# Optimization experiments

Hardware: AMD Instinct MI355X
Metric: run time of the kernel (lower is better)

## Reference

```python
import jax, jax.numpy as jnp
import numpy as np

D_MODEL = 256
D_INNER = 512
D_STATE = 16
DT_RANK = 16
D_CONV = 4
N_LAYERS = 2
EPS = 1e-5
SEQ_LEN = 16384
IN_DIM = 32
OUT_DIM = 1


def _layernorm(x, g, b):
    m = jnp.mean(x, axis=-1, keepdims=True)
    v = jnp.mean((x - m) ** 2, axis=-1, keepdims=True)
    return (x - m) * jax.lax.rsqrt(v + EPS) * g + b


def _rmsnorm(x, w):
    return x * jax.lax.rsqrt(jnp.mean(x * x, axis=-1, keepdims=True) + EPS) * w


def _selective_scan(x, delta, A, B, C, D):
    # x, delta: (B,L,ED); A: (ED,N); B,C: (B,L,N); D: (ED,)
    dA = jnp.exp(delta[..., None] * A)                    # (B,L,ED,N)
    dBx = (delta * x)[..., None] * B[:, :, None, :]       # (B,L,ED,N)

    def comb(l, r):
        al, bl = l
        ar, br = r
        return (al * ar, bl * ar + br)

    _, hs = jax.lax.associative_scan(comb, (dA, dBx), axis=1)  # (B,L,ED,N)
    y = jnp.einsum('blen,bln->ble', hs, C) + x * D
    return y


def _mamba_block(u, rms_w, inW, convW, convB, xpW, dtW, dtB, A_log, Dp, outW):
    h = _rmsnorm(u, rms_w)
    xz = h @ inW                                   # (B,L,2*ED)
    xin, z = jnp.split(xz, 2, axis=-1)
    # depthwise causal conv1d over time
    xc = jax.lax.conv_general_dilated(
        jnp.transpose(xin, (0, 2, 1)), convW,
        window_strides=(1,), padding=[(D_CONV - 1, 0)],
        feature_group_count=D_INNER,
        dimension_numbers=('NCH', 'OIH', 'NCH')) + convB[None, :, None]
    xs = jax.nn.silu(jnp.transpose(xc, (0, 2, 1)))  # (B,L,ED)
    dbc = xs @ xpW                                  # (B,L,dt_rank+2N)
    delta = jax.nn.softplus(dbc[..., :DT_RANK] @ dtW + dtB)
    Bm = dbc[..., DT_RANK:DT_RANK + D_STATE]
    Cm = dbc[..., DT_RANK + D_STATE:]
    y = _selective_scan(xs, delta, -jnp.exp(A_log), Bm, Cm, Dp)
    out = (y * jax.nn.silu(z)) @ outW
    return u + out  # residual


def _forward(x, W_in, b_in, ln1_g, ln1_b,
             rms_w, inW, convW, convB, xpW, dtW, dtB, A_log, Dp, outW,
             ln2_g, ln2_b, W1, b1, ln3_g, ln3_b, W2, b2):
    # input_proj (dropout = identity in eval)
    h = jax.nn.gelu(_layernorm(x[0] @ W_in + b_in, ln1_g, ln1_b))
    h = h[None]  # (1,L,D)
    for i in range(N_LAYERS):
        h = _mamba_block(h, rms_w[i], inW[i], convW[i], convB[i], xpW[i],
                         dtW[i], dtB[i], A_log[i], Dp[i], outW[i])
    # output_proj
    h = _layernorm(h, ln2_g, ln2_b)
    h = jax.nn.gelu(h @ W1 + b1)
    h = _layernorm(h, ln3_g, ln3_b)
    h = jnp.tanh(h @ W2 + b2)
    return h.reshape(-1)


def setup_inputs() -> dict:
    key = jax.random.key(0)
    ks = jax.random.split(key, 16)
    s = 0.02
    A = jnp.tile(jnp.arange(1, D_STATE + 1, dtype=jnp.float32)[None, :], (D_INNER, 1))
    return {
        'x': jax.random.normal(ks[0], (1, SEQ_LEN, IN_DIM), jnp.float32),
        'W_in': s * jax.random.normal(ks[1], (IN_DIM, D_MODEL), jnp.float32),
        'b_in': jnp.zeros((D_MODEL,), jnp.float32),
        'ln1_g': jnp.ones((D_MODEL,), jnp.float32),
        'ln1_b': jnp.zeros((D_MODEL,), jnp.float32),
        'rms_w': jnp.ones((N_LAYERS, D_MODEL), jnp.float32),
        'inW': s * jax.random.normal(ks[2], (N_LAYERS, D_MODEL, 2 * D_INNER), jnp.float32),
        'convW': s * jax.random.normal(ks[3], (N_LAYERS, D_INNER, 1, D_CONV), jnp.float32),
        'convB': jnp.zeros((N_LAYERS, D_INNER), jnp.float32),
        'xpW': s * jax.random.normal(ks[4], (N_LAYERS, D_INNER, DT_RANK + 2 * D_STATE), jnp.float32),
        'dtW': s * jax.random.normal(ks[5], (N_LAYERS, DT_RANK, D_INNER), jnp.float32),
        'dtB': 0.1 * jax.random.normal(ks[6], (N_LAYERS, D_INNER), jnp.float32),
        'A_log': jnp.tile(jnp.log(A)[None], (N_LAYERS, 1, 1)),
        'Dp': jnp.ones((N_LAYERS, D_INNER), jnp.float32),
        'outW': s * jax.random.normal(ks[7], (N_LAYERS, D_INNER, D_MODEL), jnp.float32),
        'ln2_g': jnp.ones((D_MODEL,), jnp.float32),
        'ln2_b': jnp.zeros((D_MODEL,), jnp.float32),
        'W1': s * jax.random.normal(ks[8], (D_MODEL, D_MODEL // 2), jnp.float32),
        'b1': jnp.zeros((D_MODEL // 2,), jnp.float32),
        'ln3_g': jnp.ones((D_MODEL // 2,), jnp.float32),
        'ln3_b': jnp.zeros((D_MODEL // 2,), jnp.float32),
        'W2': s * jax.random.normal(ks[9], (D_MODEL // 2, OUT_DIM), jnp.float32),
        'b2': jnp.zeros((OUT_DIM,), jnp.float32),
    }


def reference(x, W_in, b_in, ln1_g, ln1_b, rms_w, inW, convW, convB, xpW,
              dtW, dtB, A_log, Dp, outW, ln2_g, ln2_b, W1, b1, ln3_g, ln3_b,
              W2, b2):
    return _forward(x, W_in, b_in, ln1_g, ln1_b, rms_w, inW, convW, convB,
                    xpW, dtW, dtB, A_log, Dp, outW, ln2_g, ln2_b, W1, b1,
                    ln3_g, ln3_b, W2, b2)
```

## Files before the change

### kernel.cpp

```cpp
#include <hip/hip_runtime.h>
#include <hip/hip_bf16.h>
#include <math.h>

#define L_SEQ 16384
#define DM 256
#define DI 512
#define DS 16
#define NCH 512
#define CHL 32
#define CLB 16

typedef __attribute__((ext_vector_type(8))) short short8v;
typedef __attribute__((ext_vector_type(4))) float f32x4;

__device__ __forceinline__ float tanh_fast(float x){
  float xc = fminf(x, 15.f);
  float t = __expf(2.f*xc);
  return (t-1.f)/(t+1.f);
}
__device__ __forceinline__ float gelu_f(float x){
  float x3 = x*x*x;
  return 0.5f*x*(1.0f + tanh_fast(0.7978845608028654f*(x + 0.044715f*x3)));
}
__device__ __forceinline__ float silu_f(float x){
  return x / (1.0f + __expf(-x));
}
__device__ __forceinline__ float softplus_f(float x){
  return fmaxf(x,0.0f) + __logf(1.0f + __expf(-fabsf(x)));
}
__device__ __forceinline__ float bf2f(unsigned short u){
  return __uint_as_float(((unsigned int)u)<<16);
}
__device__ __forceinline__ void gload16(const void* g, void* l){
  __builtin_amdgcn_global_load_lds((const __attribute__((address_space(1))) void*)g,
                                   (__attribute__((address_space(3))) void*)l, 16, 0, 0);
}

__device__ __forceinline__ void powers16(float r, float* dA){
  float r2 = r*r;
  float r4 = r2*r2;
  float r8 = r4*r4;
  dA[0]=r;        dA[1]=r2;       dA[2]=r2*r;     dA[3]=r4;
  dA[4]=r4*r;     dA[5]=r4*r2;    dA[6]=r4*dA[2]; dA[7]=r8;
  dA[8]=r8*r;     dA[9]=r8*r2;    dA[10]=r8*dA[2];dA[11]=r8*r4;
  dA[12]=r8*dA[4];dA[13]=r8*dA[5];dA[14]=r8*dA[6];dA[15]=r8*r8;
}

__global__ void k_prep(const float* __restrict__ inW, const float* __restrict__ rmsw,
                       const float* __restrict__ outW, const float* __restrict__ W1,
                       const float* __restrict__ xpW, const float* __restrict__ dtW,
                       __hip_bfloat16* __restrict__ inWt, __hip_bfloat16* __restrict__ outWt,
                       __hip_bfloat16* __restrict__ W1t, __hip_bfloat16* __restrict__ Wdbc_t){
  int idx = blockIdx.x*256 + threadIdx.x;
  if(idx < 524288){
    int layer = idx >> 18;
    int r = idx & 262143;
    int n = r >> 8, k = r & 255;
    inWt[idx] = __float2bfloat16(inW[layer*262144 + k*1024 + n] * rmsw[layer*256+k]);
  } else if(idx < 786432){
    int j = idx - 524288;
    int layer = j >> 17;
    int r = j & 131071;
    int n = r >> 9, k = r & 511;
    outWt[j] = __float2bfloat16(outW[layer*131072 + k*256 + n]);
  } else if(idx < 819200){
    int j = idx - 786432;
    int n = j >> 8, k = j & 255;
    W1t[j] = __float2bfloat16(W1[k*128 + n]);
  } else if(idx < 1474560){
    int j = idx - 819200;
    int layer = j / 327680;
    int r = j % 327680;
    int n = r >> 9, k = r & 511;
    const float* xp = xpW + layer*512*48;
    float v;
    if(n < 512){
      const float* dt = dtW + layer*16*512;
      float s = 0.f;
#pragma unroll
      for(int q=0;q<16;q++) s = fmaf(xp[k*48+q], dt[q*512+n], s);
      v = s;
    } else if(n < 544){
      v = xp[k*48 + 16 + (n-512)];
    } else v = 0.f;
    Wdbc_t[j] = __float2bfloat16(v);
  }
}

__global__ void k_zero(float* __restrict__ p){
  ((float4*)p)[blockIdx.x*256 + threadIdx.x] = make_float4(0.f,0.f,0.f,0.f);
}

__global__ __launch_bounds__(256) void k_input(const float* __restrict__ x,
                        const float* __restrict__ Win, const float* __restrict__ bin,
                        const float* __restrict__ g, const float* __restrict__ b,
                        __hip_bfloat16* __restrict__ u, float* __restrict__ rowsq){
  int wv = threadIdx.x>>6, lane = threadIdx.x&63;
  int r = blockIdx.x*4 + wv;
  int c0 = lane*4;
  float acc[4];
  { float4 bv = *(const float4*)&bin[c0];
    acc[0]=bv.x; acc[1]=bv.y; acc[2]=bv.z; acc[3]=bv.w; }
#pragma unroll
  for(int k=0;k<32;k++){
    float xk = x[r*32+k];
    float4 wv4 = *(const float4*)&Win[k*DM+c0];
    acc[0]=fmaf(xk,wv4.x,acc[0]); acc[1]=fmaf(xk,wv4.y,acc[1]);
    acc[2]=fmaf(xk,wv4.z,acc[2]); acc[3]=fmaf(xk,wv4.w,acc[3]);
  }
  float s = (acc[0]+acc[1])+(acc[2]+acc[3]);
  float sq = acc[0]*acc[0]+acc[1]*acc[1]+acc[2]*acc[2]+acc[3]*acc[3];
#pragma unroll
  for(int o=32;o;o>>=1){ s += __shfl_xor(s,o); sq += __shfl_xor(sq,o); }
  float mean = s*(1.0f/DM);
  float var = sq*(1.0f/DM) - mean*mean;
  float rs = rsqrtf(var+1e-5f);
  float4 gv = *(const float4*)&g[c0];
  float4 bv = *(const float4*)&b[c0];
  float go[4];
  go[0] = gelu_f((acc[0]-mean)*rs*gv.x+bv.x);
  go[1] = gelu_f((acc[1]-mean)*rs*gv.y+bv.y);
  go[2] = gelu_f((acc[2]-mean)*rs*gv.z+bv.z);
  go[3] = gelu_f((acc[3]-mean)*rs*gv.w+bv.w);
  float ssq = go[0]*go[0]+go[1]*go[1]+go[2]*go[2]+go[3]*go[3];
#pragma unroll
  for(int o=32;o;o>>=1) ssq += __shfl_xor(ssq,o);
  if(lane==0) rowsq[r] = ssq;
  __hip_bfloat16 ob[4] = {__float2bfloat16(go[0]),__float2bfloat16(go[1]),
                          __float2bfloat16(go[2]),__float2bfloat16(go[3])};
  *(uint2*)&u[r*DM+c0] = *(uint2*)ob;
}

__global__ __launch_bounds__(256) void k_ln(const __hip_bfloat16* __restrict__ u,
                     const float* __restrict__ g, const float* __restrict__ b,
                     __hip_bfloat16* __restrict__ o){
  int wv = threadIdx.x>>6, lane = threadIdx.x&63;
  int r = blockIdx.x*4 + wv;
  int c0 = lane*4;
  ushort4 uv = *(const ushort4*)&u[r*DM+c0];
  float v[4] = {bf2f(uv.x), bf2f(uv.y), bf2f(uv.z), bf2f(uv.w)};
  float s = (v[0]+v[1])+(v[2]+v[3]);
  float sq = v[0]*v[0]+v[1]*v[1]+v[2]*v[2]+v[3]*v[3];
#pragma unroll
  for(int o2=32;o2;o2>>=1){ s += __shfl_xor(s,o2); sq += __shfl_xor(sq,o2); }
  float mean = s*(1.0f/DM);
  float var = sq*(1.0f/DM) - mean*mean;
  float rs = rsqrtf(var+1e-5f);
  float4 gv = *(const float4*)&g[c0];
  float4 bv = *(const float4*)&b[c0];
  __hip_bfloat16 ob[4] = {
    __float2bfloat16((v[0]-mean)*rs*gv.x+bv.x),
    __float2bfloat16((v[1]-mean)*rs*gv.y+bv.y),
    __float2bfloat16((v[2]-mean)*rs*gv.z+bv.z),
    __float2bfloat16((v[3]-mean)*rs*gv.w+bv.w)};
  *(uint2*)&o[r*DM+c0] = *(uint2*)ob;
}

template<int EPI, typename OT>
__global__ __launch_bounds__(512) void k_mgemm(const __hip_bfloat16* __restrict__ A,
    const __hip_bfloat16* __restrict__ Wt, const float* __restrict__ bias,
    const OT* __restrict__ R, OT* __restrict__ C, float* __restrict__ C2,
    float* __restrict__ rowsq, int M, int K, int ldc, int Nout){
  __shared__ char lds[69632];
  short* As = (short*)lds;
  short* Bs = (short*)(lds + 32768);
  float* Ob = (float*)lds;
  int t = threadIdx.x, lane = t&63, wave = t>>6;
  int gx = gridDim.x;
  int f = blockIdx.y*gx + blockIdx.x;
  int s = f >> 3;
  int sy = s/gx;
  int yb = (f&7)*(gridDim.y>>3) + sy;
  int xb = s - sy*gx;
  int m0 = yb*128, n0 = xb*128;
  int wm = (wave>>1)*32, wn = (wave&1)*64;
  f32x4 acc[2][4] = {};
  int nk = K >> 7;
  for(int ki=0; ki<nk; ki++){
    int kt = ki<<7;
    __syncthreads();
#pragma unroll
    for(int c=0;c<4;c++){
      int off = c*8192 + t*16;
      int row = off>>8;
      int sl  = ((off>>4)&15) ^ (row&15);
      gload16(&A [(m0+row)*K + kt + sl*8], (char*)As + off);
      gload16(&Wt[(n0+row)*K + kt + sl*8], (char*)Bs + off);
    }
    asm volatile("s_waitcnt vmcnt(0)" ::: "memory");
    __syncthreads();
#pragma unroll
    for(int ks=0; ks<4; ks++){
      short8v a[2], b[4];
      int k8 = ks*4 + (lane>>4);
#pragma unroll
      for(int i=0;i<2;i++){
        int lr = wm + i*16 + (lane&15);
        a[i] = *(const short8v*)&As[lr*128 + (k8 ^ (lr&15))*8];
      }
#pragma unroll
      for(int j=0;j<4;j++){
        int lr = wn + j*16 + (lane&15);
        b[j] = *(const short8v*)&Bs[lr*128 + (k8 ^ (lr&15))*8];
      }
#pragma unroll
      for(int i=0;i<2;i++)
#pragma unroll
        for(int j=0;j<4;j++)
          acc[i][j] = __builtin_amdgcn_mfma_f32_16x16x32_bf16(a[i], b[j], acc[i][j], 0,0,0);
    }
  }
  __syncthreads();
#pragma unroll
  for(int i=0;i<2;i++){
    int r0 = wm + i*16 + (lane>>4)*4;
#pragma unroll
    for(int j=0;j<4;j++){
      int cl = wn + j*16 + (lane&15);
#pragma unroll
      for(int r=0;r<4;r++) Ob[(r0+r)*132 + cl] = acc[i][j][r];
    }
  }
  __syncthreads();
  float ssq_acc = 0.f;
  int rowq = t>>2;
  int growq = m0 + rowq;
#pragma unroll
  for(int v=0; v<8; v++){
    int fidx = (t*8+v)*4;
    int row = fidx>>7, col = fidx&127;
    if(col < Nout){
      float4 o = *(const float4*)&Ob[row*132 + col];
      int grow = m0 + row, gcol = n0 + col;
      if(EPI==1 || EPI==5){
        if constexpr(sizeof(OT)==2){
          ushort4 rv = *(const ushort4*)&R[grow*ldc+gcol];
          o.x+=bf2f(rv.x); o.y+=bf2f(rv.y); o.z+=bf2f(rv.z); o.w+=bf2f(rv.w);
        } else {
          float4 rv = *(const float4*)&R[grow*ldc+gcol];
          o.x+=rv.x; o.y+=rv.y; o.z+=rv.z; o.w+=rv.w;
        }
        if(EPI==5) ssq_acc += o.x*o.x + o.y*o.y + o.z*o.z + o.w*o.w;
      }
      if(EPI==2){
        float4 bv = *(const float4*)&bias[gcol];
        o.x=gelu_f(o.x+bv.x); o.y=gelu_f(o.y+bv.y);
        o.z=gelu_f(o.z+bv.z); o.w=gelu_f(o.w+bv.w);
      }
      if(EPI==6){
        float rs = rsqrtf(rowsq[grow]*(1.0f/DM) + 1e-5f);
        o.x*=rs; o.y*=rs; o.z*=rs; o.w*=rs;
      }
      if(EPI==4){
        if(gcol < 512){
          float4 bv = *(const float4*)&bias[gcol];
          float4 so = {softplus_f(o.x+bv.x), softplus_f(o.y+bv.y),
                       softplus_f(o.z+bv.z), softplus_f(o.w+bv.w)};
          __hip_bfloat16 ob[4] = {__float2bfloat16(so.x),__float2bfloat16(so.y),
                                  __float2bfloat16(so.z),__float2bfloat16(so.w)};
          *(uint2*)&C[grow*ldc+gcol] = *(uint2*)ob;
        } else {
          *(float4*)&C2[grow*32 + (gcol-512)] = o;
        }
      } else {
        if constexpr(sizeof(OT)==2){
          __hip_bfloat16 ob[4] = {__float2bfloat16(o.x),__float2bfloat16(o.y),
                                  __float2bfloat16(o.z),__float2bfloat16(o.w)};
          *(uint2*)&C[grow*ldc+gcol] = *(uint2*)ob;
        } else {
          *(float4*)&C[grow*ldc+gcol] = o;
        }
      }
    }
  }
  if(EPI==5){
    ssq_acc += __shfl_xor(ssq_acc,1);
    ssq_acc += __shfl_xor(ssq_acc,2);
    if((lane&3)==0) atomicAdd(&rowsq[growq], ssq_acc);
  }
}

__global__ __launch_bounds__(256) void k_conv(const __hip_bfloat16* __restrict__ xz,
                       const float* __restrict__ cw, const float* __restrict__ cb,
                       __hip_bfloat16* __restrict__ xs_bf){
  int idx = blockIdx.x*256 + threadIdx.x;
  int cg = idx & 127, lb = idx >> 7;
  int c4 = cg*4;
  int l0 = lb*CLB;
  float w[4][4], bias[4];
#pragma unroll
  for(int j=0;j<4;j++){
    float4 wv = *(const float4*)&cw[(c4+j)*4];
    w[j][0]=wv.x; w[j][1]=wv.y; w[j][2]=wv.z; w[j][3]=wv.w;
  }
  { float4 bv = *(const float4*)&cb[c4];
    bias[0]=bv.x; bias[1]=bv.y; bias[2]=bv.z; bias[3]=bv.w; }
  float xm0[4], xm1[4], xm2[4];
#pragma unroll
  for(int j=0;j<4;j++){ xm0[j]=0.f; xm1[j]=0.f; xm2[j]=0.f; }
  if(l0 >= 3){
    ushort4 r0 = *(const ushort4*)&xz[(l0-3)*1024 + c4];
    ushort4 r1 = *(const ushort4*)&xz[(l0-2)*1024 + c4];
    ushort4 r2 = *(const ushort4*)&xz[(l0-1)*1024 + c4];
    xm0[0]=bf2f(r0.x); xm0[1]=bf2f(r0.y); xm0[2]=bf2f(r0.z); xm0[3]=bf2f(r0.w);
    xm1[0]=bf2f(r1.x); xm1[1]=bf2f(r1.y); xm1[2]=bf2f(r1.z); xm1[3]=bf2f(r1.w);
    xm2[0]=bf2f(r2.x); xm2[1]=bf2f(r2.y); xm2[2]=bf2f(r2.z); xm2[3]=bf2f(r2.w);
  }
#pragma unroll 4
  for(int l=l0; l<l0+CLB; l++){
    ushort4 rc = *(const ushort4*)&xz[l*1024 + c4];
    float xc[4] = {bf2f(rc.x), bf2f(rc.y), bf2f(rc.z), bf2f(rc.w)};
    __hip_bfloat16 ob[4];
#pragma unroll
    for(int j=0;j<4;j++){
      float acc = bias[j];
      acc = fmaf(xm0[j], w[j][0], acc);
      acc = fmaf(xm1[j], w[j][1], acc);
      acc = fmaf(xm2[j], w[j][2], acc);
      acc = fmaf(xc[j],  w[j][3], acc);
      ob[j] = __float2bfloat16(silu_f(acc));
    }
    *(uint2*)&xs_bf[l*DI + c4] = *(uint2*)ob;
#pragma unroll
    for(int j=0;j<4;j++){ xm0[j]=xm1[j]; xm1[j]=xm2[j]; xm2[j]=xc[j]; }
  }
}

__global__ __launch_bounds__(256) void k_scan1(const __hip_bfloat16* __restrict__ delta,
                        const __hip_bfloat16* __restrict__ xs,
                        const float* __restrict__ dbc32, const float* __restrict__ A_log,
                        float* __restrict__ Atot, float* __restrict__ Btot){
  __shared__ float bcs[CHL*32];
  int t = threadIdx.x;
  int chunk = blockIdx.x >> 1;
  int e = ((blockIdx.x & 1) << 8) + t;
  int l0 = chunk*CHL;
  ((float4*)bcs)[t] = ((const float4*)&dbc32[l0*32])[t];
  float A[16];
  {
    const float4* al = (const float4*)&A_log[e*DS];
#pragma unroll
    for(int q=0;q<4;q++){
      float4 a = al[q];
      A[q*4+0] = -__expf(a.x); A[q*4+1] = -__expf(a.y);
      A[q*4+2] = -__expf(a.z); A[q*4+3] = -__expf(a.w);
    }
  }
  bool pf = true;
#pragma unroll
  for(int n=1;n<16;n++) pf = pf && (fabsf(A[n] - (n+1)*A[0]) <= 1e-4f*fabsf(A[n]));
  float carry[16], aprod[16];
#pragma unroll
  for(int n=0;n<16;n++){ carry[n]=0.f; aprod[n]=1.f; }
  __syncthreads();
  if(pf){
    float A0 = A[0];
#pragma unroll 2
    for(int li=0; li<CHL; li++){
      int l = l0 + li;
      float d  = bf2f(*(const unsigned short*)&delta[l*DI+e]);
      float xv = bf2f(*(const unsigned short*)&xs[l*DI+e]);
      float dxv = d*xv;
      const float4* bp = (const float4*)&bcs[li*32];
      float4 b0=bp[0], b1=bp[1], b2=bp[2], b3=bp[3];
      float B[16] = {b0.x,b0.y,b0.z,b0.w, b1.x,b1.y,b1.z,b1.w,
                     b2.x,b2.y,b2.z,b2.w, b3.x,b3.y,b3.z,b3.w};
      float r = __expf(d*A0);
      float dA[16]; powers16(r, dA);
#pragma unroll
      for(int n=0;n<16;n++){
        carry[n] = fmaf(carry[n], dA[n], dxv*B[n]);
        aprod[n] *= dA[n];
      }
    }
  } else {
#pragma unroll 2
    for(int li=0; li<CHL; li++){
      int l = l0 + li;
      float d  = bf2f(*(const unsigned short*)&delta[l*DI+e]);
      float xv = bf2f(*(const unsigned short*)&xs[l*DI+e]);
      float dxv = d*xv;
      const float4* bp = (const float4*)&bcs[li*32];
      float4 b0=bp[0], b1=bp[1], b2=bp[2], b3=bp[3];
      float B[16] = {b0.x,b0.y,b0.z,b0.w, b1.x,b1.y,b1.z,b1.w,
                     b2.x,b2.y,b2.z,b2.w, b3.x,b3.y,b3.z,b3.w};
#pragma unroll
      for(int n=0;n<16;n++){
        float dA = __expf(d*A[n]);
        carry[n] = fmaf(carry[n], dA, dxv*B[n]);
        aprod[n] *= dA;
      }
    }
  }
  float4* ap = (float4*)&Atot[chunk*8192 + e*DS];
  float4* bp = (float4*)&Btot[chunk*8192 + e*DS];
#pragma unroll
  for(int q=0;q<4;q++){
    ap[q] = make_float4(aprod[q*4],aprod[q*4+1],aprod[q*4+2],aprod[q*4+3]);
    bp[q] = make_float4(carry[q*4],carry[q*4+1],carry[q*4+2],carry[q*4+3]);
  }
}

__global__ void k_scan2(const float* __restrict__ Atot, const float* __restrict__ Btot,
                        float* __restrict__ h0){
  int tg = blockIdx.x*256 + threadIdx.x;
  float carry = 0.f;
  for(int c0=0;c0<NCH;c0+=8){
    float a[8], b[8];
#pragma unroll
    for(int j=0;j<8;j++){
      a[j] = Atot[(c0+j)*8192+tg];
      b[j] = Btot[(c0+j)*8192+tg];
    }
#pragma unroll
    for(int j=0;j<8;j++){
      h0[(c0+j)*8192+tg] = carry;
      carry = fmaf(carry, a[j], b[j]);
    }
  }
}

__global__ __launch_bounds__(256) void k_scan3(const __hip_bfloat16* __restrict__ delta,
                        const __hip_bfloat16* __restrict__ xs,
                        const float* __restrict__ dbc32, const float* __restrict__ A_log,
                        const float* __restrict__ Dp, const float* __restrict__ h0,
                        const __hip_bfloat16* __restrict__ xz, __hip_bfloat16* __restrict__ y){
  __shared__ float bcs[CHL*32];
  int t = threadIdx.x;
  int chunk = blockIdx.x >> 1;
  int e = ((blockIdx.x & 1) << 8) + t;
  int l0 = chunk*CHL;
  ((float4*)bcs)[t] = ((const float4*)&dbc32[l0*32])[t];
  float A[16];
  {
    const float4* al = (const float4*)&A_log[e*DS];
#pragma unroll
    for(int q=0;q<4;q++){
      float4 a = al[q];
      A[q*4+0] = -__expf(a.x); A[q*4+1] = -__expf(a.y);
      A[q*4+2] = -__expf(a.z); A[q*4+3] = -__expf(a.w);
    }
  }
  bool pf = true;
#pragma unroll
  for(int n=1;n<16;n++) pf = pf && (fabsf(A[n] - (n+1)*A[0]) <= 1e-4f*fabsf(A[n]));
  float carry[16];
  {
    const float4* hp = (const float4*)&h0[chunk*8192 + e*DS];
#pragma unroll
    for(int q=0;q<4;q++){
      float4 h = hp[q];
      carry[q*4+0]=h.x; carry[q*4+1]=h.y; carry[q*4+2]=h.z; carry[q*4+3]=h.w;
    }
  }
  float Dv = Dp[e];
  __syncthreads();
  if(pf){
    float A0 = A[0];
#pragma unroll 2
    for(int li=0; li<CHL; li++){
      int l = l0 + li;
      float d  = bf2f(*(const unsigned short*)&delta[l*DI+e]);
      float xv = bf2f(*(const unsigned short*)&xs[l*DI+e]);
      float dxv = d*xv;
      const float4* bp = (const float4*)&bcs[li*32];
      float4 b0=bp[0], b1=bp[1], b2=bp[2], b3=bp[3];
      float4 c0=bp[4], c1=bp[5], c2=bp[6], c3=bp[7];
      float B[16] = {b0.x,b0.y,b0.z,b0.w, b1.x,b1.y,b1.z,b1.w,
                     b2.x,b2.y,b2.z,b2.w, b3.x,b3.y,b3.z,b3.w};
      float Cv[16] = {c0.x,c0.y,c0.z,c0.w, c1.x,c1.y,c1.z,c1.w,
                      c2.x,c2.y,c2.z,c2.w, c3.x,c3.y,c3.z,c3.w};
      float r = __expf(d*A0);
      float dA[16]; powers16(r, dA);
      float p[4] = {0.f,0.f,0.f,0.f};
#pragma unroll
      for(int n=0;n<16;n++){
        carry[n] = fmaf(carry[n], dA[n], dxv*B[n]);
        p[n&3] = fmaf(carry[n], Cv[n], p[n&3]);
      }
      float ps = (p[0]+p[1]) + (p[2]+p[3]);
      float z = bf2f(*(const unsigned short*)&xz[l*1024 + 512 + e]);
      y[l*DI+e] = __float2bfloat16(fmaf(xv, Dv, ps) * silu_f(z));
    }
  } else {
#pragma unroll 2
    for(int li=0; li<CHL; li++){
      int l = l0 + li;
      float d  = bf2f(*(const unsigned short*)&delta[l*DI+e]);
      float xv = bf2f(*(const unsigned short*)&xs[l*DI+e]);
      float dxv = d*xv;
      const float4* bp = (const float4*)&bcs[li*32];
      float4 b0=bp[0], b1=bp[1], b2=bp[2], b3=bp[3];
      float4 c0=bp[4], c1=bp[5], c2=bp[6], c3=bp[7];
      float B[16] = {b0.x,b0.y,b0.z,b0.w, b1.x,b1.y,b1.z,b1.w,
                     b2.x,b2.y,b2.z,b2.w, b3.x,b3.y,b3.z,b3.w};
      float Cv[16] = {c0.x,c0.y,c0.z,c0.w, c1.x,c1.y,c1.z,c1.w,
                      c2.x,c2.y,c2.z,c2.w, c3.x,c3.y,c3.z,c3.w};
      float p[4] = {0.f,0.f,0.f,0.f};
#pragma unroll
      for(int n=0;n<16;n++){
        float dA = __expf(d*A[n]);
        carry[n] = fmaf(carry[n], dA, dxv*B[n]);
        p[n&3] = fmaf(carry[n], Cv[n], p[n&3]);
      }
      float ps = (p[0]+p[1]) + (p[2]+p[3]);
      float z = bf2f(*(const unsigned short*)&xz[l*1024 + 512 + e]);
      y[l*DI+e] = __float2bfloat16(fmaf(xv, Dv, ps) * silu_f(z));
    }
  }
}

__global__ void k_final(const float* __restrict__ h2, const float* __restrict__ g,
                        const float* __restrict__ b, const float* __restrict__ W2,
                        const float* __restrict__ b2, float* __restrict__ out){
  int lane = threadIdx.x&63;
  int wv = threadIdx.x>>6;
  int r = blockIdx.x*4 + wv;
  float v0 = h2[r*128+lane], v1 = h2[r*128+64+lane];
  float s = v0+v1, sq = v0*v0+v1*v1;
#pragma unroll
  for(int o=32;o;o>>=1){ s += __shfl_xor(s,o); sq += __shfl_xor(sq,o); }
  float mean = s*(1.0f/128), var = sq*(1.0f/128) - mean*mean;
  float rs = rsqrtf(var+1e-5f);
  float n0 = (v0-mean)*rs*g[lane]+b[lane];
  float n1 = (v1-mean)*rs*g[lane+64]+b[lane+64];
  float d = n0*W2[lane] + n1*W2[lane+64];
#pragma unroll
  for(int o=32;o;o>>=1) d += __shfl_xor(d,o);
  if(lane==0) out[r] = tanhf(d + b2[0]);
}

extern "C" void kernel_launch(void* const* d_in, const int* in_sizes, int n_in,
                              void* d_out, int out_size, void* d_ws, size_t ws_size,
                              hipStream_t stream){
  const float* x    = (const float*)d_in[0];
  const float* Win  = (const float*)d_in[1];
  const float* bin  = (const float*)d_in[2];
  const float* ln1g = (const float*)d_in[3];
  const float* ln1b = (const float*)d_in[4];
  const float* rmsw = (const float*)d_in[5];
  const float* inW  = (const float*)d_in[6];
  const float* convW= (const float*)d_in[7];
  const float* convB= (const float*)d_in[8];
  const float* xpW  = (const float*)d_in[9];
  const float* dtW  = (const float*)d_in[10];
  const float* dtB  = (const float*)d_in[11];
  const float* A_log= (const float*)d_in[12];
  const float* Dp   = (const float*)d_in[13];
  const float* outW = (const float*)d_in[14];
  const float* ln2g = (const float*)d_in[15];
  const float* ln2b = (const float*)d_in[16];
  const float* W1   = (const float*)d_in[17];
  const float* b1   = (const float*)d_in[18];
  const float* ln3g = (const float*)d_in[19];
  const float* ln3b = (const float*)d_in[20];
  const float* W2   = (const float*)d_in[21];
  const float* b2   = (const float*)d_in[22];
  float* out = (float*)d_out;
  float* ws = (float*)d_ws;
  __hip_bfloat16* u_bf = (__hip_bfloat16*)ws;
  float* rowsq0 = ws + 4194304;
  float* rowsq1 = ws + 4194304 + 16384;
  __hip_bfloat16* hn_bf = (__hip_bfloat16*)(ws + 4259840);
  __hip_bfloat16* xz_bf = (__hip_bfloat16*)(ws + 8388608);
  float* dbc32 = ws + 16777216;
  __hip_bfloat16* delta_bf = (__hip_bfloat16*)(ws + 17301504);
  __hip_bfloat16* y_bf  = (__hip_bfloat16*)(ws + 25690112);
  __hip_bfloat16* xs_bf = (__hip_bfloat16*)(ws + 29884416);
  float* Atot  = ws + 34078720;
  float* Btot  = ws + 38273024;
  float* h0    = Btot;
  float* h2    = ws;
  __hip_bfloat16* inWt   = (__hip_bfloat16*)(ws + 42467328);
  __hip_bfloat16* outWt  = (__hip_bfloat16*)(ws + 42729472);
  __hip_bfloat16* W1t    = (__hip_bfloat16*)(ws + 42860544);
  __hip_bfloat16* Wdbc_t = (__hip_bfloat16*)(ws + 42876928);

  k_prep<<<5760,256,0,stream>>>(inW, rmsw, outW, W1, xpW, dtW, inWt, outWt, W1t, Wdbc_t);
  k_zero<<<16,256,0,stream>>>(rowsq1);
  k_input<<<L_SEQ/4,256,0,stream>>>(x,Win,bin,ln1g,ln1b,u_bf,rowsq0);
  for(int i=0;i<2;i++){
    float* rsq_in = (i==0) ? rowsq0 : rowsq1;
    k_mgemm<6,__hip_bfloat16><<<dim3(8, L_SEQ/128),512,0,stream>>>(
        u_bf, inWt+i*262144, nullptr, nullptr, xz_bf, nullptr, rsq_in, L_SEQ, DM, 1024, 1024);
    k_conv<<<(L_SEQ/CLB)*128/256,256,0,stream>>>(xz_bf, convW+i*DI*4, convB+i*DI, xs_bf);
    k_mgemm<4,__hip_bfloat16><<<dim3(5, L_SEQ/128),512,0,stream>>>(
        xs_bf, Wdbc_t+i*327680, dtB+i*DI, nullptr, delta_bf, dbc32, nullptr, L_SEQ, DI, 512, 544);
    k_scan1<<<NCH*2,256,0,stream>>>(delta_bf, xs_bf, dbc32, A_log+i*DI*DS, Atot, Btot);
    k_scan2<<<32,256,0,stream>>>(Atot, Btot, h0);
    k_scan3<<<NCH*2,256,0,stream>>>(delta_bf, xs_bf, dbc32, A_log+i*DI*DS, Dp+i*DI, h0, xz_bf, y_bf);
    if(i==0){
      k_mgemm<5,__hip_bfloat16><<<dim3(2, L_SEQ/128),512,0,stream>>>(
          y_bf, outWt, nullptr, u_bf, u_bf, nullptr, rowsq1, L_SEQ, DI, 256, 256);
    } else {
      k_mgemm<1,__hip_bfloat16><<<dim3(2, L_SEQ/128),512,0,stream>>>(
          y_bf, outWt+131072, nullptr, u_bf, u_bf, nullptr, nullptr, L_SEQ, DI, 256, 256);
    }
  }
  k_ln<<<L_SEQ/4,256,0,stream>>>(u_bf, ln2g, ln2b, hn_bf);
  k_mgemm<2,float><<<dim3(1, L_SEQ/128),512,0,stream>>>(
      hn_bf, W1t, b1, nullptr, h2, nullptr, nullptr, L_SEQ, DM, 128, 128);
  k_final<<<L_SEQ/4,256,0,stream>>>(h2, ln3g, ln3b, W2, b2, out);
}
```

Baseline: 413.0 us.

## Double-buffer GEMM K-tiles and fold chunk-carry scan into scan1 tail blocks

The MFMA GEMM now uses 64-wide K tiles in two LDS buffers, so the next tile's global loads are issued before the current tile's math. It waits with a partial vmcnt plus raw barriers instead of a full drain each iteration. The epilogue is staged through LDS in two 64-row halves so the buffers fit in less shared memory. Separately, the separate k_scan2 launch is removed: the last 32 blocks of k_scan1 to finish, tracked by an atomic ticket counter, spin until all chunks are written and then run the sequential carry propagation. This saves a launch and its gap, at the cost of spin-waiting and relying on fences for cross-block visibility.

```diff
diff --git a/kernel.cpp b/kernel.cpp
--- a/kernel.cpp
+++ b/kernel.cpp
@@ -87,8 +87,9 @@
   }
 }
 
-__global__ void k_zero(float* __restrict__ p){
-  ((float4*)p)[blockIdx.x*256 + threadIdx.x] = make_float4(0.f,0.f,0.f,0.f);
+__global__ void k_zero(float* __restrict__ p, int n4){
+  int i = blockIdx.x*256 + threadIdx.x;
+  if(i < n4) ((float4*)p)[i] = make_float4(0.f,0.f,0.f,0.f);
 }
 
 __global__ __launch_bounds__(256) void k_input(const float* __restrict__ x,
@@ -161,9 +162,7 @@
     const __hip_bfloat16* __restrict__ Wt, const float* __restrict__ bias,
     const OT* __restrict__ R, OT* __restrict__ C, float* __restrict__ C2,
     float* __restrict__ rowsq, int M, int K, int ldc, int Nout){
-  __shared__ char lds[69632];
-  short* As = (short*)lds;
-  short* Bs = (short*)(lds + 32768);
+  __shared__ char lds[66560];
   float* Ob = (float*)lds;
   int t = threadIdx.x, lane = t&63, wave = t>>6;
   int gx = gridDim.x;
@@ -175,33 +174,51 @@
   int m0 = yb*128, n0 = xb*128;
   int wm = (wave>>1)*32, wn = (wave&1)*64;
   f32x4 acc[2][4] = {};
-  int nk = K >> 7;
+  int soff[2], srow[2], scol[2];
+#pragma unroll
+  for(int c=0;c<2;c++){
+    int off = c*8192 + t*16;
+    int row = off>>7;
+    int sl  = ((off>>4)&7) ^ (row&7);
+    soff[c]=off; srow[c]=row; scol[c]=sl*8;
+  }
+  int nk = K >> 6;
+#pragma unroll
+  for(int c=0;c<2;c++){
+    gload16(&A [(m0+srow[c])*K + scol[c]], lds + soff[c]);
+    gload16(&Wt[(n0+srow[c])*K + scol[c]], lds + 32768 + soff[c]);
+  }
   for(int ki=0; ki<nk; ki++){
-    int kt = ki<<7;
-    __syncthreads();
-#pragma unroll
-    for(int c=0;c<4;c++){
-      int off = c*8192 + t*16;
-      int row = off>>8;
-      int sl  = ((off>>4)&15) ^ (row&15);
-      gload16(&A [(m0+row)*K + kt + sl*8], (char*)As + off);
-      gload16(&Wt[(n0+row)*K + kt + sl*8], (char*)Bs + off);
-    }
-    asm volatile("s_waitcnt vmcnt(0)" ::: "memory");
-    __syncthreads();
-#pragma unroll
-    for(int ks=0; ks<4; ks++){
+    int co = (ki & 1) ? 16384 : 0;
+    if(ki+1 < nk){
+      int no = co ^ 16384;
+      int kt = (ki+1)<<6;
+#pragma unroll
+      for(int c=0;c<2;c++){
+        gload16(&A [(m0+srow[c])*K + kt + scol[c]], lds + no + soff[c]);
+        gload16(&Wt[(n0+srow[c])*K + kt + scol[c]], lds + 32768 + no + soff[c]);
+      }
+      asm volatile("s_waitcnt vmcnt(4)" ::: "memory");
+    } else {
+      asm volatile("s_waitcnt vmcnt(0)" ::: "memory");
+    }
+    __builtin_amdgcn_s_barrier();
+    asm volatile("" ::: "memory");
+    const short* As = (const short*)(lds + co);
+    const short* Bs = (const short*)(lds + 32768 + co);
+#pragma unroll
+    for(int ks=0; ks<2; ks++){
       short8v a[2], b[4];
       int k8 = ks*4 + (lane>>4);
 #pragma unroll
       for(int i=0;i<2;i++){
         int lr = wm + i*16 + (lane&15);
-        a[i] = *(const short8v*)&As[lr*128 + (k8 ^ (lr&15))*8];
+        a[i] = *(const short8v*)&As[lr*64 + (k8 ^ (lr&7))*8];
       }
 #pragma unroll
       for(int j=0;j<4;j++){
         int lr = wn + j*16 + (lane&15);
-        b[j] = *(const short8v*)&Bs[lr*128 + (k8 ^ (lr&15))*8];
+        b[j] = *(const short8v*)&Bs[lr*64 + (k8 ^ (lr&7))*8];
       }
 #pragma unroll
       for(int i=0;i<2;i++)
@@ -209,74 +226,78 @@
         for(int j=0;j<4;j++)
           acc[i][j] = __builtin_amdgcn_mfma_f32_16x16x32_bf16(a[i], b[j], acc[i][j], 0,0,0);
     }
-  }
-  __syncthreads();
-#pragma unroll
-  for(int i=0;i<2;i++){
-    int r0 = wm + i*16 + (lane>>4)*4;
-#pragma unroll
-    for(int j=0;j<4;j++){
-      int cl = wn + j*16 + (lane&15);
-#pragma unroll
-      for(int r=0;r<4;r++) Ob[(r0+r)*132 + cl] = acc[i][j][r];
-    }
-  }
-  __syncthreads();
-  float ssq_acc = 0.f;
-  int rowq = t>>2;
-  int growq = m0 + rowq;
-#pragma unroll
-  for(int v=0; v<8; v++){
-    int fidx = (t*8+v)*4;
-    int row = fidx>>7, col = fidx&127;
-    if(col < Nout){
-      float4 o = *(const float4*)&Ob[row*132 + col];
-      int grow = m0 + row, gcol = n0 + col;
-      if(EPI==1 || EPI==5){
-        if constexpr(sizeof(OT)==2){
-          ushort4 rv = *(const ushort4*)&R[grow*ldc+gcol];
-          o.x+=bf2f(rv.x); o.y+=bf2f(rv.y); o.z+=bf2f(rv.z); o.w+=bf2f(rv.w);
+    asm volatile("" ::: "memory");
+    __builtin_amdgcn_s_barrier();
+  }
+#pragma unroll
+  for(int h=0; h<2; h++){
+    __syncthreads();
+    if((wm>>6)==h){
+      int base = wm & 63;
+#pragma unroll
+      for(int i=0;i<2;i++)
+#pragma unroll
+        for(int j=0;j<4;j++)
+#pragma unroll
+          for(int r=0;r<4;r++)
+            Ob[(base + i*16 + (lane>>4)*4 + r)*132 + wn + j*16 + (lane&15)] = acc[i][j][r];
+    }
+    __syncthreads();
+    float ssq_acc = 0.f;
+#pragma unroll
+    for(int v=0; v<4; v++){
+      int fidx = (t*4+v)*4;
+      int row = fidx>>7, col = fidx&127;
+      if(col < Nout){
+        float4 o = *(const float4*)&Ob[row*132 + col];
+        int grow = m0 + h*64 + row, gcol = n0 + col;
+        if(EPI==1 || EPI==5){
+          if constexpr(sizeof(OT)==2){
+            ushort4 rv = *(const ushort4*)&R[grow*ldc+gcol];
+            o.x+=bf2f(rv.x); o.y+=bf2f(rv.y); o.z+=bf2f(rv.z); o.w+=bf2f(rv.w);
+          } else {
+            float4 rv = *(const float4*)&R[grow*ldc+gcol];
+            o.x+=rv.x; o.y+=rv.y; o.z+=rv.z; o.w+=rv.w;
+          }
+          if(EPI==5) ssq_acc += o.x*o.x + o.y*o.y + o.z*o.z + o.w*o.w;
+        }
+        if(EPI==2){
+          float4 bv = *(const float4*)&bias[gcol];
+          o.x=gelu_f(o.x+bv.x); o.y=gelu_f(o.y+bv.y);
+          o.z=gelu_f(o.z+bv.z); o.w=gelu_f(o.w+bv.w);
+        }
+        if(EPI==6){
+          float rs = rsqrtf(rowsq[grow]*(1.0f/DM) + 1e-5f);
+          o.x*=rs; o.y*=rs; o.z*=rs; o.w*=rs;
+        }
+        if(EPI==4){
+          if(gcol < 512){
+            float4 bv = *(const float4*)&bias[gcol];
+            float4 so = {softplus_f(o.x+bv.x), softplus_f(o.y+bv.y),
+                         softplus_f(o.z+bv.z), softplus_f(o.w+bv.w)};
+            __hip_bfloat16 ob[4] = {__float2bfloat16(so.x),__float2bfloat16(so.y),
+                                    __float2bfloat16(so.z),__float2bfloat16(so.w)};
+            *(uint2*)&C[grow*ldc+gcol] = *(uint2*)ob;
+          } else {
+            *(float4*)&C2[grow*32 + (gcol-512)] = o;
+          }
         } else {
-          float4 rv = *(const float4*)&R[grow*ldc+gcol];
-          o.x+=rv.x; o.y+=rv.y; o.z+=rv.z; o.w+=rv.w;
+          if constexpr(sizeof(OT)==2){
+            __hip_bfloat16 ob[4] = {__float2bfloat16(o.x),__float2bfloat16(o.y),
+                                    __float2bfloat16(o.z),__float2bfloat16(o.w)};
+            *(uint2*)&C[grow*ldc+gcol] = *(uint2*)ob;
+          } else {
+            *(float4*)&C[grow*ldc+gcol] = o;
+          }
         }
-        if(EPI==5) ssq_acc += o.x*o.x + o.y*o.y + o.z*o.z + o.w*o.w;
-      }
-      if(EPI==2){
-        float4 bv = *(const float4*)&bias[gcol];
-        o.x=gelu_f(o.x+bv.x); o.y=gelu_f(o.y+bv.y);
-        o.z=gelu_f(o.z+bv.z); o.w=gelu_f(o.w+bv.w);
-      }
-      if(EPI==6){
-        float rs = rsqrtf(rowsq[grow]*(1.0f/DM) + 1e-5f);
-        o.x*=rs; o.y*=rs; o.z*=rs; o.w*=rs;
-      }
-      if(EPI==4){
-        if(gcol < 512){
-          float4 bv = *(const float4*)&bias[gcol];
-          float4 so = {softplus_f(o.x+bv.x), softplus_f(o.y+bv.y),
-                       softplus_f(o.z+bv.z), softplus_f(o.w+bv.w)};
-          __hip_bfloat16 ob[4] = {__float2bfloat16(so.x),__float2bfloat16(so.y),
-                                  __float2bfloat16(so.z),__float2bfloat16(so.w)};
-          *(uint2*)&C[grow*ldc+gcol] = *(uint2*)ob;
-        } else {
-          *(float4*)&C2[grow*32 + (gcol-512)] = o;
-        }
-      } else {
-        if constexpr(sizeof(OT)==2){
-          __hip_bfloat16 ob[4] = {__float2bfloat16(o.x),__float2bfloat16(o.y),
-                                  __float2bfloat16(o.z),__float2bfloat16(o.w)};
-          *(uint2*)&C[grow*ldc+gcol] = *(uint2*)ob;
-        } else {
-          *(float4*)&C[grow*ldc+gcol] = o;
-        }
-      }
-    }
-  }
-  if(EPI==5){
-    ssq_acc += __shfl_xor(ssq_acc,1);
-    ssq_acc += __shfl_xor(ssq_acc,2);
-    if((lane&3)==0) atomicAdd(&rowsq[growq], ssq_acc);
+      }
+    }
+    if(EPI==5){
+      ssq_acc += __shfl_xor(ssq_acc,1);
+      ssq_acc += __shfl_xor(ssq_acc,2);
+      ssq_acc += __shfl_xor(ssq_acc,4);
+      if((t&7)==0) atomicAdd(&rowsq[m0 + h*64 + (t>>3)], ssq_acc);
+    }
   }
 }
 
@@ -329,7 +350,8 @@
 __global__ __launch_bounds__(256) void k_scan1(const __hip_bfloat16* __restrict__ delta,
                         const __hip_bfloat16* __restrict__ xs,
                         const float* __restrict__ dbc32, const float* __restrict__ A_log,
-                        float* __restrict__ Atot, float* __restrict__ Btot){
+                        float* __restrict__ Atot, float* __restrict__ Btot,
+                        float* __restrict__ h0, unsigned* __restrict__ ctr){
   __shared__ float bcs[CHL*32];
   int t = threadIdx.x;
   int chunk = blockIdx.x >> 1;
@@ -392,30 +414,42 @@
       }
     }
   }
-  float4* ap = (float4*)&Atot[chunk*8192 + e*DS];
-  float4* bp = (float4*)&Btot[chunk*8192 + e*DS];
-#pragma unroll
-  for(int q=0;q<4;q++){
-    ap[q] = make_float4(aprod[q*4],aprod[q*4+1],aprod[q*4+2],aprod[q*4+3]);
-    bp[q] = make_float4(carry[q*4],carry[q*4+1],carry[q*4+2],carry[q*4+3]);
-  }
-}
-
-__global__ void k_scan2(const float* __restrict__ Atot, const float* __restrict__ Btot,
-                        float* __restrict__ h0){
-  int tg = blockIdx.x*256 + threadIdx.x;
-  float carry = 0.f;
-  for(int c0=0;c0<NCH;c0+=8){
-    float a[8], b[8];
-#pragma unroll
-    for(int j=0;j<8;j++){
-      a[j] = Atot[(c0+j)*8192+tg];
-      b[j] = Btot[(c0+j)*8192+tg];
-    }
-#pragma unroll
-    for(int j=0;j<8;j++){
-      h0[(c0+j)*8192+tg] = carry;
-      carry = fmaf(carry, a[j], b[j]);
+  {
+    float4* ap = (float4*)&Atot[chunk*8192 + e*DS];
+    float4* bp = (float4*)&Btot[chunk*8192 + e*DS];
+#pragma unroll
+    for(int q=0;q<4;q++){
+      ap[q] = make_float4(aprod[q*4],aprod[q*4+1],aprod[q*4+2],aprod[q*4+3]);
+      bp[q] = make_float4(carry[q*4],carry[q*4+1],carry[q*4+2],carry[q*4+3]);
+    }
+  }
+  __threadfence();
+  __shared__ unsigned tick_s;
+  if(t==0) tick_s = atomicAdd(ctr, 1u);
+  __syncthreads();
+  unsigned tick = tick_s;
+  if(tick >= (unsigned)(NCH*2-32)){
+    if(t==0){
+      volatile unsigned* vc = (volatile unsigned*)ctr;
+      while(*vc < (unsigned)(NCH*2)) {}
+    }
+    __syncthreads();
+    __threadfence();
+    int slot = (int)tick - (NCH*2-32);
+    int tg = slot*256 + t;
+    float c2 = 0.f;
+    for(int c0=0;c0<NCH;c0+=8){
+      float a[8], b[8];
+#pragma unroll
+      for(int j=0;j<8;j++){
+        a[j] = Atot[(c0+j)*8192+tg];
+        b[j] = Btot[(c0+j)*8192+tg];
+      }
+#pragma unroll
+      for(int j=0;j<8;j++){
+        h0[(c0+j)*8192+tg] = c2;
+        c2 = fmaf(c2, a[j], b[j]);
+      }
     }
   }
 }
@@ -560,7 +594,8 @@
   float* ws = (float*)d_ws;
   __hip_bfloat16* u_bf = (__hip_bfloat16*)ws;
   float* rowsq0 = ws + 4194304;
-  float* rowsq1 = ws + 4194304 + 16384;
+  float* rowsq1 = ws + 4210688;
+  unsigned* ctr = (unsigned*)(ws + 4227072);
   __hip_bfloat16* hn_bf = (__hip_bfloat16*)(ws + 4259840);
   __hip_bfloat16* xz_bf = (__hip_bfloat16*)(ws + 8388608);
   float* dbc32 = ws + 16777216;
@@ -577,7 +612,7 @@
   __hip_bfloat16* Wdbc_t = (__hip_bfloat16*)(ws + 42876928);
 
   k_prep<<<5760,256,0,stream>>>(inW, rmsw, outW, W1, xpW, dtW, inWt, outWt, W1t, Wdbc_t);
-  k_zero<<<16,256,0,stream>>>(rowsq1);
+  k_zero<<<17,256,0,stream>>>(rowsq1, (16384+256)/4);
   k_input<<<L_SEQ/4,256,0,stream>>>(x,Win,bin,ln1g,ln1b,u_bf,rowsq0);
   for(int i=0;i<2;i++){
     float* rsq_in = (i==0) ? rowsq0 : rowsq1;
@@ -586,8 +621,7 @@
     k_conv<<<(L_SEQ/CLB)*128/256,256,0,stream>>>(xz_bf, convW+i*DI*4, convB+i*DI, xs_bf);
     k_mgemm<4,__hip_bfloat16><<<dim3(5, L_SEQ/128),512,0,stream>>>(
         xs_bf, Wdbc_t+i*327680, dtB+i*DI, nullptr, delta_bf, dbc32, nullptr, L_SEQ, DI, 512, 544);
-    k_scan1<<<NCH*2,256,0,stream>>>(delta_bf, xs_bf, dbc32, A_log+i*DI*DS, Atot, Btot);
-    k_scan2<<<32,256,0,stream>>>(Atot, Btot, h0);
+    k_scan1<<<NCH*2,256,0,stream>>>(delta_bf, xs_bf, dbc32, A_log+i*DI*DS, Atot, Btot, h0, ctr+i);
     k_scan3<<<NCH*2,256,0,stream>>>(delta_bf, xs_bf, dbc32, A_log+i*DI*DS, Dp+i*DI, h0, xz_bf, y_bf);
     if(i==0){
       k_mgemm<5,__hip_bfloat16><<<dim3(2, L_SEQ/128),512,0,stream>>>(
```

After: 688.5 us. 1.67x slower.
